# Kernel optimization log

Hardware: AMD Instinct MI355X
Metric: run time of the kernel (lower is better)

The kernel has to match this reference:

```python
import jax, jax.numpy as jnp
import numpy as np

B, LQ, LK = 128, 512, 512
QS, KS, AS = 256, 256, 64


def setup_inputs() -> dict:
    key = jax.random.key(0)
    ks = jax.random.split(key, 7)
    s = 0.05
    return {
        "queries": jax.random.normal(ks[0], (B, LQ, QS), dtype=jnp.float32),
        "keys": jax.random.normal(ks[1], (B, LK, KS), dtype=jnp.float32),
        "w_relation": jax.random.normal(ks[2], (QS, KS), dtype=jnp.float32) * s,
        "W_q": jax.random.normal(ks[3], (QS, AS), dtype=jnp.float32) * s,
        "W_k": jax.random.normal(ks[4], (KS, AS), dtype=jnp.float32) * s,
        "W_q_att": jax.random.normal(ks[5], (AS, 1), dtype=jnp.float32) * s,
        "W_k_att": jax.random.normal(ks[6], (AS, 1), dtype=jnp.float32) * s,
    }


def reference(queries, keys, w_relation, W_q, W_k, W_q_att, W_k_att):
    # relation_scores: [B, Lq, Lk]
    rel = jnp.tanh(jnp.einsum("bqd,de,bke->bqk", queries, w_relation, keys))
    q_proj = jnp.einsum("bqd,da->bqa", queries, W_q)   # [B, Lq, A]
    k_proj = jnp.einsum("bkd,da->bka", keys, W_k)      # [B, Lk, A]
    q_att_score = jnp.tanh(q_proj + jnp.einsum("bqk,bka->bqa", rel, k_proj))
    k_att_score = jnp.tanh(k_proj + jnp.einsum("bqk,bqa->bka", rel, q_proj))
    # softmax over the sequence dim (dim=1)
    q_att_w = jax.nn.softmax(q_att_score @ W_q_att, axis=1)  # [B, Lq, 1]
    k_att_w = jax.nn.softmax(k_att_score @ W_k_att, axis=1)  # [B, Lk, 1]
    weighted_queries = q_att_w * queries
    weighted_keys = k_att_w * keys
    return (weighted_queries, weighted_keys, q_att_w, k_att_w)
```

## Files before the change

### kernel.cpp

```cpp
#include <hip/hip_runtime.h>
#include <math.h>


#define SEQ 512
#define DIM 256
#define ADIM 64
#define OUT_QATT ((size_t)33554432)

using hfrag = __attribute__((ext_vector_type(8))) _Float16;
using s4 = __attribute__((ext_vector_type(4))) short;
using f4 = __attribute__((ext_vector_type(4))) float;
typedef unsigned int u32;

__device__ __forceinline__ void gl_lds16(const short* g, short* l) {
  __builtin_amdgcn_global_load_lds((const __attribute__((address_space(1))) u32*)g,
                                   (__attribute__((address_space(3))) u32*)l, 16, 0, 0);
}

__device__ __forceinline__ short f2h(float x) {
  _Float16 h = (_Float16)x;
  return __builtin_bit_cast(short, h);
}
__device__ __forceinline__ float h2f(short s) {
  return (float)__builtin_bit_cast(_Float16, s);
}
__device__ __forceinline__ float tanhf_fast(float x) {
  float e = __expf(2.0f * x);
  return 1.0f - 2.0f / (e + 1.0f);
}


template <int KTOT>
__device__ __forceinline__ void core128(const short* __restrict__ A,
                                        const short* __restrict__ Bt,
                                        short* sA, short* sB, f4 acc[4][4]) {
  const int t = threadIdx.x;
  const int lane = t & 63, wave = t >> 6;
  const int wm = (wave & 1) << 6, wn = (wave >> 1) << 6;
  const int l15 = lane & 15, qd = lane >> 4;
  const int srow = t >> 3, scol = (t & 7) << 3;
  for (int k0 = 0; k0 < KTOT; k0 += 64) {
#pragma unroll
    for (int i = 0; i < 4; i++) {
      const int row = srow + (i << 5);
      const int gcol = k0 + (scol ^ ((row & 7) << 3));
      gl_lds16(&A[(size_t)row * KTOT + gcol], &sA[t * 8 + i * 2048]);
      gl_lds16(&Bt[(size_t)row * KTOT + gcol], &sB[t * 8 + i * 2048]);
    }
    __syncthreads();
#pragma unroll
    for (int ks = 0; ks < 2; ks++) {
      hfrag af[4], bg[4];
      const int kk = (ks << 5) + (qd << 3);
#pragma unroll
      for (int i = 0; i < 4; i++) {
        const int ar = wm + (i << 4) + l15;
        const int br = wn + (i << 4) + l15;
        af[i] = *(const hfrag*)&sA[(ar << 6) + (kk ^ ((ar & 7) << 3))];
        bg[i] = *(const hfrag*)&sB[(br << 6) + (kk ^ ((br & 7) << 3))];
      }
#pragma unroll
      for (int i = 0; i < 4; i++)
#pragma unroll
        for (int j = 0; j < 4; j++)
          acc[i][j] = __builtin_amdgcn_mfma_f32_16x16x32_f16(af[i], bg[j], acc[i][j], 0, 0, 0);
    }
    __syncthreads();
  }
}

template <int KTOT>
__device__ __forceinline__ void core64(const short* __restrict__ A,
                                       const short* __restrict__ Bt,
                                       short* sA, short* sB, f4 acc[4][2]) {
  const int t = threadIdx.x;
  const int lane = t & 63, wave = t >> 6;
  const int wm = (wave & 1) << 6, wn = (wave >> 1) << 5;
  const int l15 = lane & 15, qd = lane >> 4;
  const int srow = t >> 3, scol = (t & 7) << 3;
  for (int k0 = 0; k0 < KTOT; k0 += 64) {
#pragma unroll
    for (int i = 0; i < 4; i++) {
      const int row = srow + (i << 5);
      const int gcol = k0 + (scol ^ ((row & 7) << 3));
      gl_lds16(&A[(size_t)row * KTOT + gcol], &sA[t * 8 + i * 2048]);
      if (i < 2) gl_lds16(&Bt[(size_t)row * KTOT + gcol], &sB[t * 8 + i * 2048]);
    }
    __syncthreads();
#pragma unroll
    for (int ks = 0; ks < 2; ks++) {
      hfrag af[4], bg[2];
      const int kk = (ks << 5) + (qd << 3);
#pragma unroll
      for (int i = 0; i < 4; i++) {
        const int ar = wm + (i << 4) + l15;
        af[i] = *(const hfrag*)&sA[(ar << 6) + (kk ^ ((ar & 7) << 3))];
      }
#pragma unroll
      for (int j = 0; j < 2; j++) {
        const int br = wn + (j << 4) + l15;
        bg[j] = *(const hfrag*)&sB[(br << 6) + (kk ^ ((br & 7) << 3))];
      }
#pragma unroll
      for (int i = 0; i < 4; i++)
#pragma unroll
        for (int j = 0; j < 2; j++)
          acc[i][j] = __builtin_amdgcn_mfma_f32_16x16x32_f16(af[i], bg[j], acc[i][j], 0, 0, 0);
    }
    __syncthreads();
  }
}


__global__ __launch_bounds__(256) void cvt_kernel(const float* __restrict__ Q,
                                                  const float* __restrict__ K,
                                                  const float* __restrict__ wrel,
                                                  const float* __restrict__ Wq,
                                                  const float* __restrict__ Wk,
                                                  short* __restrict__ Qh, short* __restrict__ Kh,
                                                  short* __restrict__ wrelT,
                                                  short* __restrict__ WqT,
                                                  short* __restrict__ WkT) {
  const int bid = blockIdx.x;
  if (bid < 32768) {
    const size_t g = ((size_t)bid << 8) + threadIdx.x;
    const int side = (int)(g >> 22);
    const size_t loc = g & 4194303;
    const float4 v = ((const float4*)(side ? K : Q))[loc];
    s4 o;
    o[0] = f2h(v.x); o[1] = f2h(v.y); o[2] = f2h(v.z); o[3] = f2h(v.w);
    *(s4*)&(side ? Kh : Qh)[loc << 2] = o;
  } else {
    const int b2 = bid - 32768;
    if (b2 < 64) {
      const int i = (b2 << 8) + threadIdx.x;
#pragma unroll
      for (int u = 0; u < 4; u++) {
        const int idx = (i << 2) + u;
        const int e = idx >> 8, d = idx & 255;
        wrelT[idx] = f2h(wrel[(d << 8) + e]);
      }
    } else if (b2 < 72) {
      const int i = ((b2 - 64) << 8) + threadIdx.x;
#pragma unroll
      for (int u = 0; u < 8; u++) {
        const int idx = (i << 3) + u;
        const int a = idx >> 8, d = idx & 255;
        WqT[idx] = f2h(Wq[(d << 6) + a]);
      }
    } else if (b2 < 80) {
      const int i = ((b2 - 72) << 8) + threadIdx.x;
#pragma unroll
      for (int u = 0; u < 8; u++) {
        const int idx = (i << 3) + u;
        const int a = idx >> 8, d = idx & 255;
        WkT[idx] = f2h(Wk[(d << 6) + a]);
      }
    }
  }
}

__global__ __launch_bounds__(256) void proj_kernel(const short* __restrict__ Qh,
                                                   const short* __restrict__ Kh,
                                                   const short* __restrict__ WqT,
                                                   const short* __restrict__ WkT,
                                                   short* __restrict__ qp, short* __restrict__ kp,
                                                   short* __restrict__ qpT, short* __restrict__ kpT) {
  __shared__ short sA[8192];
  __shared__ short sB[4096];
  const int which = blockIdx.y;
  const short* A = which ? Kh : Qh;
  const short* Bt = which ? WkT : WqT;
  short* P = which ? kp : qp;
  short* PT = which ? kpT : qpT;
  const int m0 = blockIdx.x << 7;
  f4 acc[4][2];
  const f4 fz = {0.f, 0.f, 0.f, 0.f};
#pragma unroll
  for (int i = 0; i < 4; i++)
#pragma unroll
    for (int j = 0; j < 2; j++) acc[i][j] = fz;
  core64<256>(A + (size_t)m0 * 256, Bt, sA, sB, acc);
  const int lane = threadIdx.x & 63, wave = threadIdx.x >> 6;
  const int wm = (wave & 1) << 6, wn = (wave >> 1) << 5;
  const int l15 = lane & 15, qd = lane >> 4;
#pragma unroll
  for (int i = 0; i < 4; i++)
#pragma unroll
    for (int j = 0; j < 2; j++) {
      s4 pack;
      const int gm0 = m0 + wm + (i << 4) + (qd << 2);
      const int a = wn + (j << 4) + l15;
#pragma unroll
      for (int r = 0; r < 4; r++) {
        pack[r] = f2h(acc[i][j][r]);
        P[(size_t)(gm0 + r) * ADIM + a] = pack[r];
      }
      const int bb = gm0 >> 9, ql = gm0 & 511;
      *(s4*)&PT[((size_t)bb * ADIM + a) * SEQ + ql] = pack;
    }
}

__global__ __launch_bounds__(256) void qw_kernel(const short* __restrict__ Qh,
                                                 const short* __restrict__ WrT,
                                                 short* __restrict__ qw) {
  __shared__ short sA[8192];
  __shared__ short sB[8192];
  const int m0 = blockIdx.x << 7, n0 = blockIdx.y << 7;
  f4 acc[4][4];
  const f4 fz = {0.f, 0.f, 0.f, 0.f};
#pragma unroll
  for (int i = 0; i < 4; i++)
#pragma unroll
    for (int j = 0; j < 4; j++) acc[i][j] = fz;
  core128<256>(Qh + (size_t)m0 * 256, WrT + (size_t)n0 * 256, sA, sB, acc);
  const int lane = threadIdx.x & 63, wave = threadIdx.x >> 6;
  const int wm = (wave & 1) << 6, wn = (wave >> 1) << 6;
  const int l15 = lane & 15, qd = lane >> 4;
#pragma unroll
  for (int i = 0; i < 4; i++)
#pragma unroll
    for (int j = 0; j < 4; j++)
#pragma unroll
      for (int r = 0; r < 4; r++) {
        const int row = m0 + wm + (i << 4) + (qd << 2) + r;
        const int col = n0 + wn + (j << 4) + l15;
        qw[(size_t)row * 256 + col] = f2h(acc[i][j][r]);
      }
}

__global__ __launch_bounds__(256, 4) void side_kernel(const short* __restrict__ qw,
                                                      const short* __restrict__ Kh,
                                                      const short* __restrict__ qpT,
                                                      const short* __restrict__ kpT,
                                                      const short* __restrict__ qp,
                                                      const short* __restrict__ kp,
                                                      const float* __restrict__ Wqa,
                                                      const float* __restrict__ Wka,
                                                      float* __restrict__ qlog,
                                                      float* __restrict__ klog) {
  __shared__ short sA[16384];
  __shared__ short sB[8192];
  const int sideK = blockIdx.z;
  const short* Asrc = sideK ? Kh : qw;
  const short* Bsrc = sideK ? qw : Kh;
  const short* pT = sideK ? qpT : kpT;
  const short* prow = sideK ? kp : qp;
  const float* Watt = sideK ? Wka : Wqa;
  float* logit = sideK ? klog : qlog;

  const int tt = blockIdx.x;
  const int b = blockIdx.y;
  const int t = threadIdx.x;
  const int lane = t & 63, wave = t >> 6;
  const int l15 = lane & 15, qd = lane >> 4;
  const int wm = (wave & 1) << 5, wn = (wave >> 1) << 6;
  const f4 fz = {0.f, 0.f, 0.f, 0.f};

  {
    const short* Ag = Asrc + ((size_t)b * SEQ + tt * 64) * DIM;
    const int chunk = t & 31;
    const int rb = t >> 5;
#pragma unroll
    for (int i = 0; i < 8; i++) {
      const int row = (i << 3) + rb;
      const int gcol = (chunk << 3) ^ ((row & 7) << 3);
      gl_lds16(&Ag[(size_t)row * DIM + gcol], &sA[(row << 8) + (chunk << 3)]);
    }
  }

  f4 pacc[4];
#pragma unroll
  for (int j = 0; j < 4; j++) pacc[j] = fz;

  const short* pT_b = pT + (size_t)b * ADIM * SEQ;
  const int srow = t >> 3, scol = (t & 7) << 3;

  for (int n0 = 0; n0 < 4; n0++) {
    f4 acc[2][4];
#pragma unroll
    for (int i = 0; i < 2; i++)
#pragma unroll
      for (int j = 0; j < 4; j++) acc[i][j] = fz;
    const short* Bg = Bsrc + ((size_t)b * SEQ + n0 * 128) * DIM;
    for (int k0 = 0; k0 < 256; k0 += 64) {
#pragma unroll
      for (int i = 0; i < 4; i++) {
        const int row = srow + (i << 5);
        const int gcol = k0 + (scol ^ ((row & 7) << 3));
        gl_lds16(&Bg[(size_t)row * DIM + gcol], &sB[t * 8 + i * 2048]);
      }
      __syncthreads();
#pragma unroll
      for (int ks = 0; ks < 2; ks++) {
        const int kkB = (ks << 5) + (qd << 3);
        const int kkA = k0 + kkB;
        hfrag af[2], bg[4];
#pragma unroll
        for (int i = 0; i < 2; i++) {
          const int ar = wm + (i << 4) + l15;
          af[i] = *(const hfrag*)&sA[(ar << 8) + (kkA ^ ((ar & 7) << 3))];
        }
#pragma unroll
        for (int j = 0; j < 4; j++) {
          const int br = wn + (j << 4) + l15;
          bg[j] = *(const hfrag*)&sB[(br << 6) + (kkB ^ ((br & 7) << 3))];
        }
#pragma unroll
        for (int i = 0; i < 2; i++)
#pragma unroll
          for (int j = 0; j < 4; j++)
            acc[i][j] = __builtin_amdgcn_mfma_f32_16x16x32_f16(af[i], bg[j], acc[i][j], 0, 0, 0);
      }
      __syncthreads();
    }
#pragma unroll
    for (int i = 0; i < 2; i++)
#pragma unroll
      for (int j = 0; j < 4; j++) {
        const int row0 = wm + (i << 4) + (qd << 2);
        const int col = wn + (j << 4) + l15;
#pragma unroll
        for (int r = 0; r < 4; r++) {
          const int row = row0 + r;
          sB[(row << 7) + (col ^ ((row & 7) << 3))] = f2h(tanhf_fast(acc[i][j][r]));
        }
      }
    __syncthreads();
#pragma unroll
    for (int ks = 0; ks < 4; ks++) {
      const int kkk = (ks << 5) + (qd << 3);
      const int ar = (wave << 4) + l15;
      const hfrag aq = *(const hfrag*)&sB[(ar << 7) + (kkk ^ ((ar & 7) << 3))];
#pragma unroll
      for (int j2 = 0; j2 < 4; j2++) {
        const int a = (j2 << 4) + l15;
        const hfrag bq = *(const hfrag*)&pT_b[(size_t)a * SEQ + (n0 << 7) + kkk];
        pacc[j2] = __builtin_amdgcn_mfma_f32_16x16x32_f16(aq, bq, pacc[j2], 0, 0, 0);
      }
    }
    __syncthreads();
  }

  const int row_l = (wave << 4) + (qd << 2);
  const size_t g0 = (size_t)b * SEQ + tt * 64 + row_l;
  float p[4] = {0.f, 0.f, 0.f, 0.f};
#pragma unroll
  for (int r = 0; r < 4; r++)
#pragma unroll
    for (int j2 = 0; j2 < 4; j2++) {
      const int a = (j2 << 4) + l15;
      p[r] += tanhf_fast(h2f(prow[(g0 + r) * ADIM + a]) + pacc[j2][r]) * Watt[a];
    }
#pragma unroll
  for (int off = 8; off; off >>= 1)
#pragma unroll
    for (int r = 0; r < 4; r++) p[r] += __shfl_down(p[r], off, 16);
  if (l15 == 0) {
#pragma unroll
    for (int r = 0; r < 4; r++) logit[g0 + r] = p[r];
  }
}

__global__ __launch_bounds__(256) void softmax_kernel(const float* __restrict__ qlog,
                                                      const float* __restrict__ klog,
                                                      float* __restrict__ out) {
  const int bx = blockIdx.x;
  const int side = bx >> 7;
  const int b = bx & 127;
  const float* lg = (side ? klog : qlog) + (size_t)b * SEQ;
  float* o = out + OUT_QATT + (size_t)side * (128 * SEQ) + (size_t)b * SEQ;
  const int t = threadIdx.x;
  float v0 = lg[t];
  float v1 = lg[t + 256];
  float m = fmaxf(v0, v1);
#pragma unroll
  for (int off = 32; off; off >>= 1) m = fmaxf(m, __shfl_xor(m, off));
  __shared__ float sm[4], ss[4];
  const int w = t >> 6, l = t & 63;
  if (l == 0) sm[w] = m;
  __syncthreads();
  m = fmaxf(fmaxf(sm[0], sm[1]), fmaxf(sm[2], sm[3]));
  float e0 = expf(v0 - m), e1 = expf(v1 - m);
  float s = e0 + e1;
#pragma unroll
  for (int off = 32; off; off >>= 1) s += __shfl_xor(s, off);
  if (l == 0) ss[w] = s;
  __syncthreads();
  s = ss[0] + ss[1] + ss[2] + ss[3];
  float inv = 1.0f / s;
  o[t] = e0 * inv;
  o[t + 256] = e1 * inv;
}

__global__ __launch_bounds__(256) void weight_kernel(const float* __restrict__ queries,
                                                     const float* __restrict__ keys,
                                                     float* __restrict__ out) {
  const size_t g = (size_t)blockIdx.x * 256 + threadIdx.x;
  const int side = (int)(g >> 22);
  const size_t loc = g & 4194303;
  const size_t row = loc >> 6;
  const float* aw = out + OUT_QATT + (size_t)side * (128 * SEQ);
  const float4* src = (const float4*)(side ? keys : queries);
  const float w = aw[row];
  float4 v = src[loc];
  float4 r = {v.x * w, v.y * w, v.z * w, v.w * w};
  ((float4*)out)[g] = r;
}

extern "C" void kernel_launch(void* const* d_in, const int* in_sizes, int n_in,
                              void* d_out, int out_size, void* d_ws, size_t ws_size,
                              hipStream_t stream) {
  const float* queries = (const float*)d_in[0];
  const float* keys = (const float*)d_in[1];
  const float* w_rel = (const float*)d_in[2];
  const float* W_q = (const float*)d_in[3];
  const float* W_k = (const float*)d_in[4];
  const float* W_qa = (const float*)d_in[5];
  const float* W_ka = (const float*)d_in[6];
  float* out = (float*)d_out;

  short* Qh = (short*)d_ws;
  short* Kh = Qh + 16777216;
  short* qp = Kh + 16777216;
  short* kp = qp + 4194304;
  float* qlog = (float*)(kp + 4194304);
  float* klog = qlog + 65536;

  char* ob = (char*)d_out;
  short* qw_s = (short*)ob;
  short* qpT = (short*)(ob + 100663296);
  short* kpT = (short*)(ob + 109051904);
  short* wrelT = (short*)(ob + 117440512);
  short* WqT = (short*)(ob + 117571584);
  short* WkT = (short*)(ob + 117604352);

  cvt_kernel<<<32848, 256, 0, stream>>>(queries, keys, w_rel, W_q, W_k, Qh, Kh, wrelT, WqT, WkT);
  proj_kernel<<<dim3(512, 2), 256, 0, stream>>>(Qh, Kh, WqT, WkT, qp, kp, qpT, kpT);
  qw_kernel<<<dim3(512, 2), 256, 0, stream>>>(Qh, wrelT, qw_s);
  side_kernel<<<dim3(8, 128, 2), 256, 0, stream>>>(qw_s, Kh, qpT, kpT, qp, kp, W_qa, W_ka, qlog, klog);
  softmax_kernel<<<256, 256, 0, stream>>>(qlog, klog, out);
  weight_kernel<<<32768, 256, 0, stream>>>(queries, keys, out);
}
```

Before: 442.8 us.

## Read B operand directly from global in side_kernel and remap grid for L2 locality

The side kernel stops staging the B tile through LDS with async global-to-LDS copies and instead loads MFMA B fragments straight from global memory, which removes two barriers per k-step. The grid is flattened to 1D and remapped so that the blocks sharing a batch and side (the 8 row tiles) are scheduled close together, with the XCD interleave in mind, to improve L2 reuse of the shared B matrix. A barrier after the A load and a removed trailing barrier adjust synchronisation. The risk is more global traffic and higher latency on the uncoalesced 16-byte B fragment loads.

```diff
diff --git a/kernel.cpp b/kernel.cpp
--- a/kernel.cpp
+++ b/kernel.cpp
@@ -240,8 +240,13 @@
                                                       float* __restrict__ qlog,
                                                       float* __restrict__ klog) {
   __shared__ short sA[16384];
-  __shared__ short sB[8192];
-  const int sideK = blockIdx.z;
+  __shared__ short sT[8192];
+  const int i = blockIdx.x;
+  const int pair = ((i >> 6) << 3) | (i & 7);
+  const int tt = (i >> 3) & 7;
+  const int b = pair >> 1;
+  const int sideK = pair & 1;
+
   const short* Asrc = sideK ? Kh : qw;
   const short* Bsrc = sideK ? qw : Kh;
   const short* pT = sideK ? qpT : kpT;
@@ -249,8 +254,6 @@
   const float* Watt = sideK ? Wka : Wqa;
   float* logit = sideK ? klog : qlog;
 
-  const int tt = blockIdx.x;
-  const int b = blockIdx.y;
   const int t = threadIdx.x;
   const int lane = t & 63, wave = t >> 6;
   const int l15 = lane & 15, qd = lane >> 4;
@@ -262,68 +265,61 @@
     const int chunk = t & 31;
     const int rb = t >> 5;
 #pragma unroll
-    for (int i = 0; i < 8; i++) {
-      const int row = (i << 3) + rb;
+    for (int u = 0; u < 8; u++) {
+      const int row = (u << 3) + rb;
       const int gcol = (chunk << 3) ^ ((row & 7) << 3);
       gl_lds16(&Ag[(size_t)row * DIM + gcol], &sA[(row << 8) + (chunk << 3)]);
     }
   }
+  __syncthreads();
 
   f4 pacc[4];
 #pragma unroll
   for (int j = 0; j < 4; j++) pacc[j] = fz;
 
   const short* pT_b = pT + (size_t)b * ADIM * SEQ;
-  const int srow = t >> 3, scol = (t & 7) << 3;
 
   for (int n0 = 0; n0 < 4; n0++) {
     f4 acc[2][4];
 #pragma unroll
-    for (int i = 0; i < 2; i++)
-#pragma unroll
-      for (int j = 0; j < 4; j++) acc[i][j] = fz;
+    for (int i2 = 0; i2 < 2; i2++)
+#pragma unroll
+      for (int j = 0; j < 4; j++) acc[i2][j] = fz;
     const short* Bg = Bsrc + ((size_t)b * SEQ + n0 * 128) * DIM;
+#pragma unroll
     for (int k0 = 0; k0 < 256; k0 += 64) {
 #pragma unroll
-      for (int i = 0; i < 4; i++) {
-        const int row = srow + (i << 5);
-        const int gcol = k0 + (scol ^ ((row & 7) << 3));
-        gl_lds16(&Bg[(size_t)row * DIM + gcol], &sB[t * 8 + i * 2048]);
-      }
-      __syncthreads();
-#pragma unroll
       for (int ks = 0; ks < 2; ks++) {
-        const int kkB = (ks << 5) + (qd << 3);
-        const int kkA = k0 + kkB;
+        const int kkA = k0 + (ks << 5) + (qd << 3);
         hfrag af[2], bg[4];
 #pragma unroll
-        for (int i = 0; i < 2; i++) {
-          const int ar = wm + (i << 4) + l15;
-          af[i] = *(const hfrag*)&sA[(ar << 8) + (kkA ^ ((ar & 7) << 3))];
+        for (int i2 = 0; i2 < 2; i2++) {
+          const int ar = wm + (i2 << 4) + l15;
+          af[i2] = *(const hfrag*)&sA[(ar << 8) + (kkA ^ ((ar & 7) << 3))];
         }
 #pragma unroll
         for (int j = 0; j < 4; j++) {
           const int br = wn + (j << 4) + l15;
-          bg[j] = *(const hfrag*)&sB[(br << 6) + (kkB ^ ((br & 7) << 3))];
+          bg[j] = *(const hfrag*)&Bg[(size_t)br * DIM + kkA];
         }
 #pragma unroll
-        for (int i = 0; i < 2; i++)
+        for (int i2 = 0; i2 < 2; i2++)
 #pragma unroll
           for (int j = 0; j < 4; j++)
-            acc[i][j] = __builtin_amdgcn_mfma_f32_16x16x32_f16(af[i], bg[j], acc[i][j], 0, 0, 0);
-      }
-      __syncthreads();
-    }
-#pragma unroll
-    for (int i = 0; i < 2; i++)
+            acc[i2][j] = __builtin_amdgcn_mfma_f32_16x16x32_f16(af[i2], bg[j], acc[i2][j], 0, 0, 0);
+      }
+    }
+    __syncthreads();
+#pragma unroll
+    for (int i2 = 0; i2 < 2; i2++)
 #pragma unroll
       for (int j = 0; j < 4; j++) {
-        const int row0 = wm + (i << 4) + (qd << 2);
+        const int row0 = wm + (i2 << 4) + (qd << 2);
         const int col = wn + (j << 4) + l15;
 #pragma unroll
         for (int r = 0; r < 4; r++) {
           const int row = row0 + r;
-          sB[(row << 7) + (col ^ ((row & 7) << 3))] = f2h(tanhf_fast(acc[i][j][r]));
+          sT[(row << 7) + (col ^ ((row & 7) << 3))] = f2h(tanhf_fast(acc[i2][j][r]));
         }
       }
     __syncthreads();
@@ -331,7 +327,7 @@
     for (int ks = 0; ks < 4; ks++) {
       const int kkk = (ks << 5) + (qd << 3);
       const int ar = (wave << 4) + l15;
-      const hfrag aq = *(const hfrag*)&sB[(ar << 7) + (kkk ^ ((ar & 7) << 3))];
+      const hfrag aq = *(const hfrag*)&sT[(ar << 7) + (kkk ^ ((ar & 7) << 3))];
 #pragma unroll
       for (int j2 = 0; j2 < 4; j2++) {
         const int a = (j2 << 4) + l15;
@@ -339,7 +335,6 @@
         pacc[j2] = __builtin_amdgcn_mfma_f32_16x16x32_f16(aq, bq, pacc[j2], 0, 0, 0);
       }
     }
-    __syncthreads();
   }
 
   const int row_l = (wave << 4) + (qd << 2);
@@ -438,7 +433,7 @@
   cvt_kernel<<<32848, 256, 0, stream>>>(queries, keys, w_rel, W_q, W_k, Qh, Kh, wrelT, WqT, WkT);
   proj_kernel<<<dim3(512, 2), 256, 0, stream>>>(Qh, Kh, WqT, WkT, qp, kp, qpT, kpT);
   qw_kernel<<<dim3(512, 2), 256, 0, stream>>>(Qh, wrelT, qw_s);
-  side_kernel<<<dim3(8, 128, 2), 256, 0, stream>>>(qw_s, Kh, qpT, kpT, qp, kp, W_qa, W_ka, qlog, klog);
+  side_kernel<<<2048, 256, 0, stream>>>(qw_s, Kh, qpT, kpT, qp, kp, W_qa, W_ka, qlog, klog);
   softmax_kernel<<<256, 256, 0, stream>>>(qlog, klog, out);
   weight_kernel<<<32768, 256, 0, stream>>>(queries, keys, out);
 }
```

Result: slower. 508.6 us (+14.9%).
